# Kernel optimization log

Measured on AMD Instinct MI355X. Metric: run time of the kernel, lower is better.

Reference implementation:

```python
import jax, jax.numpy as jnp
import numpy as np

BS, SEQ, D_IN, D_OUT = 4, 1024, 1024, 1024
N_SKILLS, RANK = 8, 4
SCALING = 1.0  # lora_alpha / rank, folded into one constant
NEG_INF = -1e38


def setup_inputs() -> dict:
    key = jax.random.key(0)
    ks = jax.random.split(key, 5)
    x = jax.random.normal(ks[0], (BS, SEQ, D_IN), jnp.float32)
    phi = jax.random.normal(ks[1], (D_IN, N_SKILLS), jnp.float32) * 0.02
    lora_a = jax.random.normal(ks[2], (N_SKILLS, D_IN, RANK), jnp.float32) * 0.02
    lora_b = jax.random.normal(ks[3], (N_SKILLS, RANK, D_OUT), jnp.float32) * 0.02
    W = jax.random.normal(ks[4], (D_OUT, D_IN), jnp.float32) * 0.02
    b = jnp.zeros((D_OUT,), jnp.float32)
    # left-padded sequences with an instruction prefix right after the padding
    pad_len = np.array([100, 0, 250, 50])
    inst_len = 300
    pad = np.zeros((BS, SEQ), np.int32)
    inst = np.zeros((BS, SEQ), np.int32)
    for i in range(BS):
        pad[i, pad_len[i]:] = 1
        inst[i, pad_len[i]:pad_len[i] + inst_len] = 1
    return {"x": x, "phi": phi, "lora_a": lora_a, "lora_b": lora_b,
            "W": W, "b": b,
            "inst_mask": jnp.asarray(inst), "pad_mask": jnp.asarray(pad)}


def _causal_prefix_mask(inst_mask, pad_mask):
    # faithful port of create_causal_prefix_mask (padding_side='left')
    bs, seq = inst_mask.shape
    first_one = jnp.argmax(inst_mask, axis=1, keepdims=True)          # [b,1]
    n_ones = jnp.sum(inst_mask, axis=1, keepdims=True)                # [b,1]
    thresh = first_one + n_ones                                       # last_one_idx + 1
    exp = jnp.broadcast_to(thresh, (bs, seq))                         # [b,s]
    inv = jnp.maximum(seq - exp - jnp.arange(seq)[None, :], 0)[:, ::-1]
    m = (exp + inv) * pad_mask                                        # [b,s]
    m3 = m[:, :, None] * pad_mask[:, None, :]                         # [b,s,s]
    ar = jnp.arange(seq)[None, None, :]
    return ar < m3                                                    # bool [b,s,s]


def reference(x, phi, lora_a, lora_b, W, b, inst_mask, pad_mask):
    # router: mixing logits per token per skill
    mw = jnp.einsum('bsd,dn->bsn', x, phi)                            # [b,s,k]
    cm = _causal_prefix_mask(inst_mask, pad_mask)                     # [b,s,s]
    padf = pad_mask.astype(x.dtype)
    # expand over attended positions p, mask, softmax over p
    logits = jnp.where(cm[..., None], mw[:, :, None, :], NEG_INF)     # [b,s,p,k]
    logits = jnp.transpose(logits, (0, 3, 1, 2))                      # [b,k,s,p]
    D = jax.nn.softmax(logits, axis=-1)
    D = D * padf[:, None, :, None]                                    # zero padded query rows
    # token mixing: contract over source tokens (last axis of D)
    input_mixed = jnp.einsum('bsd,bkps->bkpd', x, D)                  # [b,k,s,d]
    # per-skill LoRA (n_splits == 1, q squeezed)
    ar_r = jnp.einsum('bksd,kdr->bskr', input_mixed, lora_a)          # [b,s,k,r]
    ad = jnp.einsum('bskr,krd->bskd', ar_r, lora_b)                   # [b,s,k,d_out]
    # softmax-weighted combine over skills
    C = jax.nn.softmax(mw, axis=-1)
    adapter_out = jnp.einsum('bsk,bskd->bsd', C, ad) * SCALING
    base = jnp.einsum('bsd,od->bso', x, W) + b
    return base + adapter_out
```

## Files before the change

kernel.cpp:

```cpp
#include <hip/hip_runtime.h>
#include <hip/hip_bf16.h>
#include <cstdint>

#define SEQ   1024
#define DOUT  1024
#define KDIM  1024
#define MTOT  4096
#define WCROWS 1104

typedef __bf16 bf16x8 __attribute__((ext_vector_type(8)));
typedef float  f32x4  __attribute__((ext_vector_type(4)));

__device__ inline unsigned short f2bf(float f) {
  union { float f; unsigned u; } a; a.f = f;
  unsigned r = a.u + 0x7fff + ((a.u >> 16) & 1);
  return (unsigned short)(r >> 16);
}

__device__ inline void gl16(const void* g, void* l) {
  __builtin_amdgcn_global_load_lds((__attribute__((address_space(1))) void*)g,
                                   (__attribute__((address_space(3))) void*)l, 16, 0, 0);
}

__global__ __launch_bounds__(256) void k_cvt_x(const float4* __restrict__ x, ushort4* __restrict__ xb) {
  int i = blockIdx.x * 256 + threadIdx.x;
  float4 v = x[i];
  ushort4 o; o.x = f2bf(v.x); o.y = f2bf(v.y); o.z = f2bf(v.z); o.w = f2bf(v.w);
  xb[i] = o;
}

__global__ __launch_bounds__(256) void k_build_wc(const float* __restrict__ W, const float* __restrict__ phi,
                                                  const float* __restrict__ la, const float* __restrict__ lb,
                                                  unsigned short* __restrict__ Wc) {
  int i = blockIdx.x * 256 + threadIdx.x;
  int row = i >> 10, d = i & 1023;
  float v;
  if (row < 1024)       v = W[i];
  else if (row < 1032)  v = phi[d * 8 + (row - 1024)];
  else if (row < 1064)  { int kr = row - 1032; v = la[(kr >> 2) * 4096 + d * 4 + (kr & 3)]; }
  else if (row < 1072)  v = 0.f;
  else                  v = lb[(row - 1072) * 1024 + d];
  Wc[i] = f2bf(v);
}

__global__ __launch_bounds__(256) void k_mwz(const unsigned short* __restrict__ xb,
                                             const unsigned short* __restrict__ Wc,
                                             float* __restrict__ mwzT) {
  __shared__ unsigned short As[64 * 32];
  __shared__ unsigned short Bs[48 * 32];
  int bm = blockIdx.x;
  int t = threadIdx.x, wave = t >> 6, lane = t & 63;
  int quad = lane >> 4, lr = lane & 15;
  f32x4 acc[3];
#pragma unroll
  for (int i = 0; i < 3; ++i) acc[i] = (f32x4){0.f, 0.f, 0.f, 0.f};
  const unsigned short* aG = xb + (size_t)bm * 64 * KDIM;
  const unsigned short* bG = Wc + (size_t)1024 * KDIM;
  int r0 = t >> 2, c0 = (t & 3) * 8;
  for (int kb = 0; kb < KDIM; kb += 32) {
    __syncthreads();
    gl16(aG + (size_t)r0 * KDIM + kb + c0, &As[wave * 512]);
    if (t < 192) gl16(bG + (size_t)r0 * KDIM + kb + c0, &Bs[wave * 512]);
    __syncthreads();
    bf16x8 af = *(const bf16x8*)&As[(wave * 16 + lr) * 32 + quad * 8];
#pragma unroll
    for (int ni = 0; ni < 3; ++ni) {
      bf16x8 bfr = *(const bf16x8*)&Bs[(ni * 16 + lr) * 32 + quad * 8];
      acc[ni] = __builtin_amdgcn_mfma_f32_16x16x32_bf16(af, bfr, acc[ni], 0, 0, 0);
    }
  }
#pragma unroll
  for (int ni = 0; ni < 3; ++ni) {
    int c = ni * 16 + lr;
#pragma unroll
    for (int rg = 0; rg < 4; ++rg) {
      int row = bm * 64 + wave * 16 + quad * 4 + rg;
      if (c < 40) mwzT[(size_t)c * MTOT + row] = acc[ni][rg];
    }
  }
}

__global__ __launch_bounds__(1024) void k_scan(const float* __restrict__ mwzT,
                                               const int* __restrict__ inst, const int* __restrict__ pad,
                                               float* __restrict__ T, float* __restrict__ Pc,
                                               int* __restrict__ thr) {
  int b = blockIdx.x, c = blockIdx.y;
  int tid = threadIdx.x;
  int wv = tid >> 6, lane = tid & 63;
  __shared__ float ws[16];
  __shared__ int fos[16], nos[16];

  if (c == 33) {
    int iv = inst[b * SEQ + tid];
    int fo = iv ? tid : (1 << 30);
    int no = iv;
#pragma unroll
    for (int d = 1; d < 64; d <<= 1) { fo = min(fo, __shfl_xor(fo, d)); no += __shfl_xor(no, d); }
    if (lane == 0) { fos[wv] = fo; nos[wv] = no; }
    __syncthreads();
    if (tid == 0) {
      int F = 1 << 30, N = 0;
#pragma unroll
      for (int i = 0; i < 16; ++i) { F = min(F, fos[i]); N += nos[i]; }
      thr[b] = (N > 0) ? F + N : 0;
    }
    return;
  }

  float pm = (float)pad[b * SEQ + tid];
  float v = (c < 32) ? mwzT[(size_t)(8 + c) * MTOT + b * SEQ + tid] * pm : pm;
#pragma unroll
  for (int d = 1; d < 64; d <<= 1) { float o = __shfl_up(v, d); if (lane >= d) v += o; }
  if (lane == 63) ws[wv] = v;
  __syncthreads();
  if (wv == 0 && lane < 16) {
    float orig = ws[lane], s = orig;
#pragma unroll
    for (int d = 1; d < 16; d <<= 1) { float o = __shfl_up(s, d); if (lane >= d) s += o; }
    ws[lane] = s - orig;
  }
  __syncthreads();
  v += ws[wv];
  if (c < 32) T[(size_t)c * MTOT + b * SEQ + tid] = v;
  else        Pc[b * SEQ + tid] = v;
}

__global__ __launch_bounds__(64) void k_gate(const float* __restrict__ mwzT, const float* __restrict__ T,
                                             const float* __restrict__ Pc, const int* __restrict__ thr,
                                             const int* __restrict__ pad, unsigned short* __restrict__ gb) {
  int q = blockIdx.x * 64 + threadIdx.x;
  int b = q >> 10, s = q & 1023;
  unsigned short* gp = gb + (size_t)q * 32;
  if (pad[q] == 0) {
    uint4 z4 = {0u, 0u, 0u, 0u};
#pragma unroll
    for (int i = 0; i < 4; ++i) ((uint4*)gp)[i] = z4;
    return;
  }
  int e = max(thr[b], s + 1) - 1;
  int e0 = b * SEQ + e;
  float cnt = Pc[e0];
  float C[8], mx = -1e30f;
#pragma unroll
  for (int k = 0; k < 8; ++k) { C[k] = mwzT[(size_t)k * MTOT + q]; mx = fmaxf(mx, C[k]); }
  float sm = 0.f;
#pragma unroll
  for (int k = 0; k < 8; ++k) { C[k] = __expf(C[k] - mx); sm += C[k]; }
  float inv = 1.f / (sm * cnt);
#pragma unroll
  for (int kr = 0; kr < 32; ++kr)
    gp[kr] = f2bf(C[kr >> 2] * inv * T[(size_t)kr * MTOT + e0]);
}

__global__ __launch_bounds__(256) void k_gemm(const unsigned short* __restrict__ A,
                                              const unsigned short* __restrict__ Wc,
                                              const unsigned short* __restrict__ gb,
                                              float* __restrict__ out,
                                              const float* __restrict__ bias) {
  __shared__ unsigned short As[128 * 32];
  __shared__ unsigned short Bs[64 * 32];
  int bm = blockIdx.x, bn = blockIdx.y;
  int t = threadIdx.x;
  int wave = t >> 6, lane = t & 63;
  int wr = wave >> 1, wc = wave & 1;
  int quad = lane >> 4, lr = lane & 15;
  f32x4 acc[4][2];
#pragma unroll
  for (int i = 0; i < 4; i++)
#pragma unroll
    for (int j = 0; j < 2; j++) acc[i][j] = (f32x4){0.f, 0.f, 0.f, 0.f};

  const unsigned short* aG = A + (size_t)bm * 128 * KDIM;
  const unsigned short* bG = Wc + (size_t)bn * 64 * KDIM;
  int r0 = t >> 2, c0 = (t & 3) * 8;

  for (int kb = 0; kb < KDIM; kb += 32) {
    __syncthreads();
    gl16(aG + (size_t)r0 * KDIM + kb + c0, &As[wave * 512]);
    gl16(aG + (size_t)(r0 + 64) * KDIM + kb + c0, &As[2048 + wave * 512]);
    gl16(bG + (size_t)r0 * KDIM + kb + c0, &Bs[wave * 512]);
    __syncthreads();
    bf16x8 af[4], bfr[2];
#pragma unroll
    for (int mi = 0; mi < 4; mi++) af[mi]  = *(const bf16x8*)&As[(wr * 64 + mi * 16 + lr) * 32 + quad * 8];
#pragma unroll
    for (int ni = 0; ni < 2; ni++) bfr[ni] = *(const bf16x8*)&Bs[(wc * 32 + ni * 16 + lr) * 32 + quad * 8];
#pragma unroll
    for (int mi = 0; mi < 4; mi++)
#pragma unroll
      for (int ni = 0; ni < 2; ni++)
        acc[mi][ni] = __builtin_amdgcn_mfma_f32_16x16x32_bf16(af[mi], bfr[ni], acc[mi][ni], 0, 0, 0);
  }

  __syncthreads();
  gl16(gb + (size_t)(bm * 128 + r0) * 32 + c0,        &As[wave * 512]);
  gl16(gb + (size_t)(bm * 128 + 64 + r0) * 32 + c0,   &As[2048 + wave * 512]);
  {
    int kr = t >> 3, co = (t & 7) * 8;
    uint4 v = *(const uint4*)(Wc + (size_t)(1072 + kr) * KDIM + bn * 64 + co);
    *(uint4*)&Bs[kr * 64 + co] = v;
  }
  __syncthreads();
  bf16x8 af2[4];
#pragma unroll
  for (int mi = 0; mi < 4; mi++) af2[mi] = *(const bf16x8*)&As[(wr * 64 + mi * 16 + lr) * 32 + quad * 8];
#pragma unroll
  for (int ni = 0; ni < 2; ni++) {
    union { bf16x8 v; unsigned short u[8]; } bu;
    int col = wc * 32 + ni * 16 + lr;
#pragma unroll
    for (int j = 0; j < 8; ++j) bu.u[j] = Bs[(quad * 8 + j) * 64 + col];
#pragma unroll
    for (int mi = 0; mi < 4; mi++)
      acc[mi][ni] = __builtin_amdgcn_mfma_f32_16x16x32_bf16(af2[mi], bu.v, acc[mi][ni], 0, 0, 0);
  }

#pragma unroll
  for (int mi = 0; mi < 4; mi++) {
#pragma unroll
    for (int ni = 0; ni < 2; ni++) {
      int col = bn * 64 + wc * 32 + ni * 16 + lr;
      float bv = bias[col];
#pragma unroll
      for (int rg = 0; rg < 4; ++rg) {
        int row = bm * 128 + wr * 64 + mi * 16 + quad * 4 + rg;
        out[(size_t)row * DOUT + col] = acc[mi][ni][rg] + bv;
      }
    }
  }
}

extern "C" void kernel_launch(void* const* d_in, const int* in_sizes, int n_in,
                              void* d_out, int out_size, void* d_ws, size_t ws_size,
                              hipStream_t stream) {
  const float* x    = (const float*)d_in[0];
  const float* phi  = (const float*)d_in[1];
  const float* la   = (const float*)d_in[2];
  const float* lb   = (const float*)d_in[3];
  const float* W    = (const float*)d_in[4];
  const float* bias = (const float*)d_in[5];
  const int*   inst = (const int*)d_in[6];
  const int*   pad  = (const int*)d_in[7];
  float* out = (float*)d_out;

  char* ws = (char*)d_ws;
  unsigned short* xb  = (unsigned short*)ws;
  unsigned short* Wc  = (unsigned short*)(ws + 8388608);
  float* mwzT = (float*)(ws + 10747904);
  float* T    = (float*)(ws + 11403264);
  float* Pc   = (float*)(ws + 11927552);
  int*   thr  = (int*)  (ws + 11943936);
  unsigned short* gb = (unsigned short*)(ws + 11948032);

  hipLaunchKernelGGL(k_cvt_x,    dim3(4096),   dim3(256),  0, stream, (const float4*)x, (ushort4*)xb);
  hipLaunchKernelGGL(k_build_wc, dim3(4416),   dim3(256),  0, stream, W, phi, la, lb, Wc);
  hipLaunchKernelGGL(k_mwz,      dim3(64),     dim3(256),  0, stream, xb, Wc, mwzT);
  hipLaunchKernelGGL(k_scan,     dim3(4, 34),  dim3(1024), 0, stream, mwzT, inst, pad, T, Pc, thr);
  hipLaunchKernelGGL(k_gate,     dim3(64),     dim3(64),   0, stream, mwzT, T, Pc, thr, pad, gb);
  hipLaunchKernelGGL(k_gemm,     dim3(32, 16), dim3(256),  0, stream, xb, Wc, gb, out, bias);
}
```

Measured before the change: 125.3 us.

## Fuse prep kernels, split-K the router GEMM, and merge scan with gating

Merges the x conversion, weight packing and instruction-threshold computation into one prep kernel. Splits the router/LoRA-A GEMM along K into 4 chunks so it runs on 256 blocks instead of 64. Fuses the prefix scan and gate computation into one kernel that sums the split-K partials, so the T and Pc intermediates are no longer written to memory. Together these cut the launch count from six to four and add parallelism to the small GEMM. In exchange the partial sums are re-read 32 times per position in the scan-gate kernel, and gb is written with scattered 2-byte stores.

```diff
diff --git a/kernel.cpp b/kernel.cpp
--- a/kernel.cpp
+++ b/kernel.cpp
@@ -22,42 +22,58 @@
                                    (__attribute__((address_space(3))) void*)l, 16, 0, 0);
 }
 
-__global__ __launch_bounds__(256) void k_cvt_x(const float4* __restrict__ x, ushort4* __restrict__ xb) {
-  int i = blockIdx.x * 256 + threadIdx.x;
-  float4 v = x[i];
-  ushort4 o; o.x = f2bf(v.x); o.y = f2bf(v.y); o.z = f2bf(v.z); o.w = f2bf(v.w);
-  xb[i] = o;
-}
-
-__global__ __launch_bounds__(256) void k_build_wc(const float* __restrict__ W, const float* __restrict__ phi,
-                                                  const float* __restrict__ la, const float* __restrict__ lb,
-                                                  unsigned short* __restrict__ Wc) {
-  int i = blockIdx.x * 256 + threadIdx.x;
-  int row = i >> 10, d = i & 1023;
-  float v;
-  if (row < 1024)       v = W[i];
-  else if (row < 1032)  v = phi[d * 8 + (row - 1024)];
-  else if (row < 1064)  { int kr = row - 1032; v = la[(kr >> 2) * 4096 + d * 4 + (kr & 3)]; }
-  else if (row < 1072)  v = 0.f;
-  else                  v = lb[(row - 1072) * 1024 + d];
-  Wc[i] = f2bf(v);
+__global__ __launch_bounds__(256) void k_prep(const float4* __restrict__ x, ushort4* __restrict__ xb,
+                                              const float* __restrict__ W, const float* __restrict__ phi,
+                                              const float* __restrict__ la, const float* __restrict__ lb,
+                                              unsigned short* __restrict__ Wc,
+                                              const int* __restrict__ inst, int* __restrict__ thr) {
+  int blk = blockIdx.x, tid = threadIdx.x;
+  if (blk < 4096) {
+    int i = blk * 256 + tid;
+    float4 v = x[i];
+    ushort4 o; o.x = f2bf(v.x); o.y = f2bf(v.y); o.z = f2bf(v.z); o.w = f2bf(v.w);
+    xb[i] = o;
+  } else if (blk < 8512) {
+    int i = (blk - 4096) * 256 + tid;
+    int row = i >> 10, d = i & 1023;
+    float v;
+    if (row < 1024)       v = W[i];
+    else if (row < 1032)  v = phi[d * 8 + (row - 1024)];
+    else if (row < 1064)  { int kr = row - 1032; v = la[(kr >> 2) * 4096 + d * 4 + (kr & 3)]; }
+    else if (row < 1072)  v = 0.f;
+    else                  v = lb[(row - 1072) * 1024 + d];
+    Wc[i] = f2bf(v);
+  } else {
+    int b = tid >> 6, lane = tid & 63;
+    int fo = 1 << 30, no = 0;
+#pragma unroll
+    for (int j = 0; j < 16; ++j) {
+      int p = j * 64 + lane;
+      int iv = inst[b * SEQ + p];
+      if (iv > 0) fo = min(fo, p);
+      no += iv;
+    }
+#pragma unroll
+    for (int d = 1; d < 64; d <<= 1) { fo = min(fo, __shfl_xor(fo, d)); no += __shfl_xor(no, d); }
+    if (lane == 0) thr[b] = (no > 0) ? fo + no : 0;
+  }
 }
 
 __global__ __launch_bounds__(256) void k_mwz(const unsigned short* __restrict__ xb,
                                              const unsigned short* __restrict__ Wc,
-                                             float* __restrict__ mwzT) {
+                                             float* __restrict__ mwzP) {
   __shared__ unsigned short As[64 * 32];
   __shared__ unsigned short Bs[48 * 32];
-  int bm = blockIdx.x;
+  int bm = blockIdx.x, ks = blockIdx.y;
   int t = threadIdx.x, wave = t >> 6, lane = t & 63;
   int quad = lane >> 4, lr = lane & 15;
   f32x4 acc[3];
 #pragma unroll
   for (int i = 0; i < 3; ++i) acc[i] = (f32x4){0.f, 0.f, 0.f, 0.f};
-  const unsigned short* aG = xb + (size_t)bm * 64 * KDIM;
-  const unsigned short* bG = Wc + (size_t)1024 * KDIM;
+  const unsigned short* aG = xb + (size_t)bm * 64 * KDIM + ks * 256;
+  const unsigned short* bG = Wc + (size_t)1024 * KDIM + ks * 256;
   int r0 = t >> 2, c0 = (t & 3) * 8;
-  for (int kb = 0; kb < KDIM; kb += 32) {
+  for (int kb = 0; kb < 256; kb += 32) {
     __syncthreads();
     gl16(aG + (size_t)r0 * KDIM + kb + c0, &As[wave * 512]);
     if (t < 192) gl16(bG + (size_t)r0 * KDIM + kb + c0, &Bs[wave * 512]);
@@ -75,81 +91,65 @@
 #pragma unroll
     for (int rg = 0; rg < 4; ++rg) {
       int row = bm * 64 + wave * 16 + quad * 4 + rg;
-      if (c < 40) mwzT[(size_t)c * MTOT + row] = acc[ni][rg];
-    }
-  }
-}
-
-__global__ __launch_bounds__(1024) void k_scan(const float* __restrict__ mwzT,
-                                               const int* __restrict__ inst, const int* __restrict__ pad,
-                                               float* __restrict__ T, float* __restrict__ Pc,
-                                               int* __restrict__ thr) {
+      if (c < 40) mwzP[(size_t)(ks * 40 + c) * MTOT + row] = acc[ni][rg];
+    }
+  }
+}
+
+__global__ __launch_bounds__(1024) void k_scan_gate(const float* __restrict__ mwzP,
+                                                    const int* __restrict__ pad, const int* __restrict__ thr,
+                                                    unsigned short* __restrict__ gb) {
   int b = blockIdx.x, c = blockIdx.y;
-  int tid = threadIdx.x;
-  int wv = tid >> 6, lane = tid & 63;
-  __shared__ float ws[16];
-  __shared__ int fos[16], nos[16];
-
-  if (c == 33) {
-    int iv = inst[b * SEQ + tid];
-    int fo = iv ? tid : (1 << 30);
-    int no = iv;
-#pragma unroll
-    for (int d = 1; d < 64; d <<= 1) { fo = min(fo, __shfl_xor(fo, d)); no += __shfl_xor(no, d); }
-    if (lane == 0) { fos[wv] = fo; nos[wv] = no; }
-    __syncthreads();
-    if (tid == 0) {
-      int F = 1 << 30, N = 0;
-#pragma unroll
-      for (int i = 0; i < 16; ++i) { F = min(F, fos[i]); N += nos[i]; }
-      thr[b] = (N > 0) ? F + N : 0;
-    }
-    return;
-  }
-
-  float pm = (float)pad[b * SEQ + tid];
-  float v = (c < 32) ? mwzT[(size_t)(8 + c) * MTOT + b * SEQ + tid] * pm : pm;
-#pragma unroll
-  for (int d = 1; d < 64; d <<= 1) { float o = __shfl_up(v, d); if (lane >= d) v += o; }
-  if (lane == 63) ws[wv] = v;
+  int tid = threadIdx.x, wv = tid >> 6, lane = tid & 63;
+  __shared__ float wsz[16], wsp[16];
+  __shared__ float sv, spc;
+  int q = b * SEQ + tid;
+  float pm = (float)pad[q];
+  float z = 0.f;
+#pragma unroll
+  for (int s = 0; s < 4; ++s) z += mwzP[(size_t)(s * 40 + 8 + c) * MTOT + q];
+  z *= pm;
+  float vz = z, vp = pm;
+#pragma unroll
+  for (int d = 1; d < 64; d <<= 1) {
+    float oz = __shfl_up(vz, d), op = __shfl_up(vp, d);
+    if (lane >= d) { vz += oz; vp += op; }
+  }
+  if (lane == 63) { wsz[wv] = vz; wsp[wv] = vp; }
   __syncthreads();
   if (wv == 0 && lane < 16) {
-    float orig = ws[lane], s = orig;
-#pragma unroll
-    for (int d = 1; d < 16; d <<= 1) { float o = __shfl_up(s, d); if (lane >= d) s += o; }
-    ws[lane] = s - orig;
-  }
-  __syncthreads();
-  v += ws[wv];
-  if (c < 32) T[(size_t)c * MTOT + b * SEQ + tid] = v;
-  else        Pc[b * SEQ + tid] = v;
-}
-
-__global__ __launch_bounds__(64) void k_gate(const float* __restrict__ mwzT, const float* __restrict__ T,
-                                             const float* __restrict__ Pc, const int* __restrict__ thr,
-                                             const int* __restrict__ pad, unsigned short* __restrict__ gb) {
-  int q = blockIdx.x * 64 + threadIdx.x;
-  int b = q >> 10, s = q & 1023;
-  unsigned short* gp = gb + (size_t)q * 32;
-  if (pad[q] == 0) {
-    uint4 z4 = {0u, 0u, 0u, 0u};
-#pragma unroll
-    for (int i = 0; i < 4; ++i) ((uint4*)gp)[i] = z4;
-    return;
-  }
-  int e = max(thr[b], s + 1) - 1;
-  int e0 = b * SEQ + e;
-  float cnt = Pc[e0];
-  float C[8], mx = -1e30f;
-#pragma unroll
-  for (int k = 0; k < 8; ++k) { C[k] = mwzT[(size_t)k * MTOT + q]; mx = fmaxf(mx, C[k]); }
-  float sm = 0.f;
-#pragma unroll
-  for (int k = 0; k < 8; ++k) { C[k] = __expf(C[k] - mx); sm += C[k]; }
-  float inv = 1.f / (sm * cnt);
-#pragma unroll
-  for (int kr = 0; kr < 32; ++kr)
-    gp[kr] = f2bf(C[kr >> 2] * inv * T[(size_t)kr * MTOT + e0]);
+    float oz = wsz[lane], op = wsp[lane], sz = oz, sp = op;
+#pragma unroll
+    for (int d = 1; d < 16; d <<= 1) {
+      float tz = __shfl_up(sz, d), tp = __shfl_up(sp, d);
+      if (lane >= d) { sz += tz; sp += tp; }
+    }
+    wsz[lane] = sz - oz; wsp[lane] = sp - op;
+  }
+  __syncthreads();
+  vz += wsz[wv]; vp += wsp[wv];
+  int th = thr[b];
+  if (th > 0 && tid == th - 1) { sv = vz; spc = vp; }
+  __syncthreads();
+  unsigned short o = 0;
+  if (pm != 0.f) {
+    bool own = (tid + 1 >= th);
+    float Tv  = own ? vz : sv;
+    float cnt = own ? vp : spc;
+    float C[8], mx = -1e30f;
+#pragma unroll
+    for (int k = 0; k < 8; ++k) {
+      float m = 0.f;
+#pragma unroll
+      for (int s = 0; s < 4; ++s) m += mwzP[(size_t)(s * 40 + k) * MTOT + q];
+      C[k] = m; mx = fmaxf(mx, m);
+    }
+    float sm = 0.f;
+#pragma unroll
+    for (int k = 0; k < 8; ++k) { C[k] = __expf(C[k] - mx); sm += C[k]; }
+    o = f2bf(C[c >> 2] * Tv / (sm * cnt));
+  }
+  gb[(size_t)q * 32 + c] = o;
 }
 
 __global__ __launch_bounds__(256) void k_gemm(const unsigned short* __restrict__ A,
@@ -246,16 +246,13 @@
   char* ws = (char*)d_ws;
   unsigned short* xb  = (unsigned short*)ws;
   unsigned short* Wc  = (unsigned short*)(ws + 8388608);
-  float* mwzT = (float*)(ws + 10747904);
-  float* T    = (float*)(ws + 11403264);
-  float* Pc   = (float*)(ws + 11927552);
-  int*   thr  = (int*)  (ws + 11943936);
-  unsigned short* gb = (unsigned short*)(ws + 11948032);
-
-  hipLaunchKernelGGL(k_cvt_x,    dim3(4096),   dim3(256),  0, stream, (const float4*)x, (ushort4*)xb);
-  hipLaunchKernelGGL(k_build_wc, dim3(4416),   dim3(256),  0, stream, W, phi, la, lb, Wc);
-  hipLaunchKernelGGL(k_mwz,      dim3(64),     dim3(256),  0, stream, xb, Wc, mwzT);
-  hipLaunchKernelGGL(k_scan,     dim3(4, 34),  dim3(1024), 0, stream, mwzT, inst, pad, T, Pc, thr);
-  hipLaunchKernelGGL(k_gate,     dim3(64),     dim3(64),   0, stream, mwzT, T, Pc, thr, pad, gb);
-  hipLaunchKernelGGL(k_gemm,     dim3(32, 16), dim3(256),  0, stream, xb, Wc, gb, out, bias);
-}
+  float* mwzP = (float*)(ws + 10649600);
+  unsigned short* gb = (unsigned short*)(ws + 13271040);
+  int*   thr  = (int*)(ws + 13533184);
+
+  hipLaunchKernelGGL(k_prep,      dim3(8513),   dim3(256),  0, stream,
+                     (const float4*)x, (ushort4*)xb, W, phi, la, lb, Wc, inst, thr);
+  hipLaunchKernelGGL(k_mwz,       dim3(64, 4),  dim3(256),  0, stream, xb, Wc, mwzP);
+  hipLaunchKernelGGL(k_scan_gate, dim3(4, 32),  dim3(1024), 0, stream, mwzP, pad, thr, gb);
+  hipLaunchKernelGGL(k_gemm,      dim3(32, 16), dim3(256),  0, stream, xb, Wc, gb, out, bias);
+}
```

New measurement: 116.7 us. 1.07x faster.
